# Kernel tuning notes

Hardware: AMD Instinct MI355X
Metric: run time of the kernel (lower is better)

The kernel has to match this reference:

```python
import jax, jax.numpy as jnp
import numpy as np

B, T, D = 8, 4096, 768
N_HEADS = 12
HEAD_DIM = D // N_HEADS
N_STATE = 64
ALPHA = 0.1


def setup_inputs() -> dict:
    key = jax.random.key(0)
    k1, k2, k3 = jax.random.split(key, 3)
    H = jax.random.normal(k1, (B, T, D), dtype=jnp.float32)
    prototypes = jax.random.normal(k2, (N_STATE, D), dtype=jnp.float32)
    W_tok = jax.random.normal(k3, (D, D), dtype=jnp.float32) * (1.0 / np.sqrt(D))
    s0 = jnp.zeros((1, N_STATE, D), dtype=jnp.float32)
    return {"H": H, "prototypes": prototypes, "W_tok": W_tok, "s0": s0}


def reference(H, prototypes, W_tok, s0):
    b, t, d = H.shape
    hd = HEAD_DIM
    a = ALPHA
    # q: [B, n_heads, T, head_dim]
    q = (H @ W_tok.T).reshape(b, t, N_HEADS, hd).transpose(0, 2, 1, 3)
    # k: [n_heads, n_state, head_dim]
    k = prototypes.reshape(N_STATE, N_HEADS, hd).transpose(1, 0, 2)
    # score: [B, n_heads, T, n_state]; routing_temp == 1.0
    score = jnp.einsum('bhtd,hmd->bhtm', q, k) / (hd ** 0.5)
    w = jax.nn.softmax(score, axis=-1)
    g = 1.0 - a * w
    # suffix-inclusive product over T: prod_{t'>=t} g[t']
    suffix_inc = jnp.flip(jnp.cumprod(jnp.flip(g, axis=2), axis=2), axis=2)
    suffix_exc = jnp.concatenate(
        [suffix_inc[:, :, 1:, :], jnp.ones_like(suffix_inc[:, :, :1, :])], axis=2)
    w_eff = a * w * suffix_exc  # [B, H, T, n_state]
    h_ph = H.reshape(b, t, N_HEADS, hd).transpose(0, 2, 1, 3)  # [B,H,T,hd]
    s0h = jnp.broadcast_to(s0, (b, N_STATE, d)).reshape(
        b, N_STATE, N_HEADS, hd).transpose(0, 2, 1, 3)  # [B,H,n_state,hd]
    residual = suffix_inc[:, :, 0, :][..., None]  # [B,H,n_state,1]
    s = s0h * residual + jnp.einsum('bhtm,bhtd->bhmd', w_eff, h_ph)
    return s.transpose(0, 2, 1, 3).reshape(b, N_STATE, d)
```

## Files before the change

kernel.cpp:

```cpp
#include <hip/hip_runtime.h>

#define B_ 8
#define T_ 4096
#define D_ 768
#define NH_ 12
#define M_ 64
#define ALPHA_ 0.1f

#define CCH 16
#define CHUNK_T 256

using half8 = __attribute__((ext_vector_type(8))) _Float16;
using short8 = __attribute__((ext_vector_type(8))) short;
using f32x4 = __attribute__((ext_vector_type(4))) float;

__device__ __forceinline__ unsigned int f2h2(float a, float b) {
    unsigned short ua = __builtin_bit_cast(unsigned short, (_Float16)a);
    unsigned short ub = __builtin_bit_cast(unsigned short, (_Float16)b);
    return (unsigned int)ua | ((unsigned int)ub << 16);
}
__device__ __forceinline__ float h2f(unsigned short u) {
    return (float)__builtin_bit_cast(_Float16, u);
}
__device__ __forceinline__ void gload_lds16(const void* g, void* l) {
    __builtin_amdgcn_global_load_lds(
        (const __attribute__((address_space(1))) unsigned int*)g,
        (__attribute__((address_space(3))) unsigned int*)l, 16, 0, 0);
}

__global__ __launch_bounds__(256) void kH16(const float* __restrict__ H,
                                            unsigned short* __restrict__ H16) {
    const int i = blockIdx.x * 256 + threadIdx.x;
#pragma unroll
    for (int j = 0; j < 4; ++j) {
        const int idx = i + j * 1572864;
        const float4 v = reinterpret_cast<const float4*>(H)[idx];
        uint2 pk = {f2h2(v.x, v.y), f2h2(v.z, v.w)};
        reinterpret_cast<uint2*>(H16)[idx] = pk;
    }
}

__global__ __launch_bounds__(256) void kP(const float* __restrict__ proto,
                                          const float* __restrict__ W,
                                          unsigned short* __restrict__ P16) {
    const int et = blockIdx.x;
    const int h  = blockIdx.y;
    const int tid = threadIdx.x;

    __shared__ __align__(16) float Ws[64 * 128];
    __shared__ __align__(16) float Ks[64 * 64];

#pragma unroll
    for (int j = 0; j < 8; ++j) {
        int f = tid + j * 256;
        int i = f >> 5, c4 = f & 31;
        const float4 v = *reinterpret_cast<const float4*>(
            W + (size_t)(h * 64 + i) * D_ + et * 128 + c4 * 4);
        *reinterpret_cast<float4*>(&Ws[i * 128 + c4 * 4]) = v;
    }
#pragma unroll
    for (int j = 0; j < 4; ++j) {
        int f = tid + j * 256;
        int m = f >> 4, i4 = f & 15;
        const float4 v = *reinterpret_cast<const float4*>(
            proto + (size_t)m * D_ + h * 64 + i4 * 4);
        Ks[(i4 * 4 + 0) * 64 + m] = v.x;
        Ks[(i4 * 4 + 1) * 64 + m] = v.y;
        Ks[(i4 * 4 + 2) * 64 + m] = v.z;
        Ks[(i4 * 4 + 3) * 64 + m] = v.w;
    }
    __syncthreads();

    const int m0 = (tid >> 5) * 8;
    const int e0 = (tid & 31) * 4;
    float acc[8][4];
#pragma unroll
    for (int i = 0; i < 8; ++i)
#pragma unroll
        for (int j = 0; j < 4; ++j) acc[i][j] = 0.f;

    for (int i = 0; i < 64; ++i) {
        const float4 bb = *reinterpret_cast<const float4*>(&Ws[i * 128 + e0]);
        const float4 a0 = *reinterpret_cast<const float4*>(&Ks[i * 64 + m0]);
        const float4 a1 = *reinterpret_cast<const float4*>(&Ks[i * 64 + m0 + 4]);
        const float a[8] = {a0.x, a0.y, a0.z, a0.w, a1.x, a1.y, a1.z, a1.w};
#pragma unroll
        for (int mi = 0; mi < 8; ++mi) {
            acc[mi][0] = fmaf(a[mi], bb.x, acc[mi][0]);
            acc[mi][1] = fmaf(a[mi], bb.y, acc[mi][1]);
            acc[mi][2] = fmaf(a[mi], bb.z, acc[mi][2]);
            acc[mi][3] = fmaf(a[mi], bb.w, acc[mi][3]);
        }
    }
#pragma unroll
    for (int mi = 0; mi < 8; ++mi) {
        size_t idx = (size_t)(h * 64 + m0 + mi) * D_ + et * 128 + e0;
        uint2 pk = {f2h2(acc[mi][0] * 0.125f, acc[mi][1] * 0.125f),
                    f2h2(acc[mi][2] * 0.125f, acc[mi][3] * 0.125f)};
        *reinterpret_cast<uint2*>(P16 + idx) = pk;
    }
}

#define LDS_BYTES 51712

__global__ __launch_bounds__(256, 3) void k1(const unsigned short* __restrict__ H16,
                                             const unsigned short* __restrict__ P16,
                                             float* __restrict__ chunkprod,
                                             float* __restrict__ partial) {
    const int p = blockIdx.x;
    const int b = p & 7;
    const int s = p >> 3;
    const int h = s % 12;
    const int c = s / 12;
    const int tid = threadIdx.x;
    const int wv  = tid >> 6;
    const int lane = tid & 63;
    const int l15 = lane & 15;
    const int q4  = lane >> 4;

    extern __shared__ __align__(16) unsigned char smem[];
    unsigned short* wT = (unsigned short*)(smem);
    unsigned short* Hh = (unsigned short*)(smem + 33792);
    float* segprod = (float*)(smem + 50688);

    const size_t Hrow = (size_t)(b * T_ + c * CHUNK_T);
    const unsigned short* gA = H16 + Hrow * D_;
    const unsigned short* gB = P16 + (size_t)h * 64 * D_;

    f32x4 acc[4][4] = {};

    for (int kt = 0; kt < 12; ++kt) {
        __syncthreads();
#pragma unroll
        for (int j = 0; j < 8; ++j) {
            int sl = j * 256 + tid;
            int r = sl >> 3, gp = sl & 7, g = gp ^ (r & 7);
            gload_lds16(gA + (size_t)r * D_ + kt * 64 + g * 8, smem + sl * 16);
        }
#pragma unroll
        for (int j = 0; j < 2; ++j) {
            int sl = j * 256 + tid;
            int r = sl >> 3, gp = sl & 7, g = gp ^ (r & 7);
            gload_lds16(gB + (size_t)r * D_ + kt * 64 + g * 8, smem + 32768 + sl * 16);
        }
        __syncthreads();
#pragma unroll
        for (int ks = 0; ks < 2; ++ks) {
            const int gp = ((ks * 4 + q4) ^ (l15 & 7)) * 16;
            half8 af[4], bf[4];
#pragma unroll
            for (int tt = 0; tt < 4; ++tt)
                af[tt] = *reinterpret_cast<const half8*>(
                    smem + (wv * 64 + tt * 16 + l15) * 128 + gp);
#pragma unroll
            for (int mt = 0; mt < 4; ++mt)
                bf[mt] = *reinterpret_cast<const half8*>(
                    smem + 32768 + (mt * 16 + l15) * 128 + gp);
#pragma unroll
            for (int tt = 0; tt < 4; ++tt)
#pragma unroll
                for (int mt = 0; mt < 4; ++mt)
                    acc[tt][mt] = __builtin_amdgcn_mfma_f32_16x16x32_f16(
                        af[tt], bf[mt], acc[tt][mt], 0, 0, 0);
        }
    }
    __syncthreads();

#pragma unroll
    for (int tt = 0; tt < 4; ++tt)
#pragma unroll
        for (int rg = 0; rg < 4; ++rg) {
            float mx = fmaxf(fmaxf(acc[tt][0][rg], acc[tt][1][rg]),
                             fmaxf(acc[tt][2][rg], acc[tt][3][rg]));
#pragma unroll
            for (int msk = 1; msk <= 8; msk <<= 1)
                mx = fmaxf(mx, __shfl_xor(mx, msk, 64));
            float e0 = __expf(acc[tt][0][rg] - mx);
            float e1 = __expf(acc[tt][1][rg] - mx);
            float e2 = __expf(acc[tt][2][rg] - mx);
            float e3 = __expf(acc[tt][3][rg] - mx);
            float sm = (e0 + e1) + (e2 + e3);
#pragma unroll
            for (int msk = 1; msk <= 8; msk <<= 1)
                sm += __shfl_xor(sm, msk, 64);
            float inv = 1.0f / sm;
            acc[tt][0][rg] = e0 * inv;
            acc[tt][1][rg] = e1 * inv;
            acc[tt][2][rg] = e2 * inv;
            acc[tt][3][rg] = e3 * inv;
        }
#pragma unroll
    for (int tt = 0; tt < 4; ++tt)
#pragma unroll
        for (int mt = 0; mt < 4; ++mt) {
            uint2 pk = {f2h2(acc[tt][mt][0], acc[tt][mt][1]),
                        f2h2(acc[tt][mt][2], acc[tt][mt][3])};
            *reinterpret_cast<uint2*>(
                wT + (mt * 16 + l15) * 264 + wv * 64 + tt * 16 + q4 * 4) = pk;
        }
    __syncthreads();

    {
        const int g = tid >> 6, m_s = tid & 63;
        unsigned short* rowp = wT + m_s * 264 + g * 64;
        float pband = 1.0f;
#pragma unroll
        for (int oct = 0; oct < 8; ++oct) {
            short8 v = *reinterpret_cast<const short8*>(rowp + oct * 8);
#pragma unroll
            for (int j = 0; j < 8; ++j)
                pband *= fmaf(-ALPHA_, h2f((unsigned short)v[j]), 1.0f);
        }
        segprod[m_s * 4 + g] = pband;
        __syncthreads();
        float R = 1.0f;
#pragma unroll
        for (int gg = 1; gg < 4; ++gg)
            if (g + gg < 4) R *= segprod[m_s * 4 + g + gg];
#pragma unroll
        for (int oct = 7; oct >= 0; --oct) {
            short8 v = *reinterpret_cast<const short8*>(rowp + oct * 8);
            short8 o;
#pragma unroll
            for (int j = 7; j >= 0; --j) {
                float w = h2f((unsigned short)v[j]);
                _Float16 we = (_Float16)(ALPHA_ * w * R);
                o[j] = (short)__builtin_bit_cast(unsigned short, we);
                R *= fmaf(-ALPHA_, w, 1.0f);
            }
            *reinterpret_cast<short8*>(rowp + oct * 8) = o;
        }
    }
    __syncthreads();

    f32x4 pacc[4] = {};
    for (int hf = 0; hf < 2; ++hf) {
        if (hf) __syncthreads();
        {
            const int dp = tid & 15, tg = tid >> 4;
            const unsigned short* src = H16 + (Hrow + tg * 16) * D_
                                        + h * 64 + hf * 32 + 2 * dp;
            unsigned short* dst0 = Hh + (2 * dp) * 264 + tg * 16;
            unsigned short* dst1 = Hh + (2 * dp + 1) * 264 + tg * 16;
#pragma unroll
            for (int i = 0; i < 16; ++i) {
                unsigned int v = *reinterpret_cast<const unsigned int*>(src + (size_t)i * D_);
                dst0[i] = (unsigned short)(v & 0xffffu);
                dst1[i] = (unsigned short)(v >> 16);
            }
        }
        __syncthreads();
#pragma unroll
        for (int ks = 0; ks < 8; ++ks) {
            half8 a = *reinterpret_cast<const half8*>(
                wT + (wv * 16 + l15) * 264 + ks * 32 + q4 * 8);
#pragma unroll
            for (int dt = 0; dt < 2; ++dt) {
                half8 bb = *reinterpret_cast<const half8*>(
                    Hh + (dt * 16 + l15) * 264 + ks * 32 + q4 * 8);
                pacc[hf * 2 + dt] = __builtin_amdgcn_mfma_f32_16x16x32_f16(
                    a, bb, pacc[hf * 2 + dt], 0, 0, 0);
            }
        }
    }

    const int chunkIdx = (b * NH_ + h) * CCH + c;
    if (tid < 64)
        chunkprod[(size_t)chunkIdx * 64 + tid] =
            (segprod[tid * 4 + 0] * segprod[tid * 4 + 1]) *
            (segprod[tid * 4 + 2] * segprod[tid * 4 + 3]);
#pragma unroll
    for (int dt = 0; dt < 4; ++dt)
#pragma unroll
        for (int rg = 0; rg < 4; ++rg)
            partial[((size_t)chunkIdx * 64 + wv * 16 + q4 * 4 + rg) * 64 + dt * 16 + l15] =
                pacc[dt][rg];
}

__global__ __launch_bounds__(256) void k2(const float* __restrict__ chunkprod,
                                          const float* __restrict__ partial,
                                          const float* __restrict__ s0,
                                          float* __restrict__ out) {
    const int h = blockIdx.x;
    const int b = blockIdx.y;
    const int mg = blockIdx.z;
    const int tid = threadIdx.x;
    const int m  = mg * 16 + (tid >> 4);
    const int d0 = (tid & 15) * 4;

    const size_t cpBase = (size_t)(b * NH_ + h) * CCH;
    float sfx[CCH];
    float run = 1.0f;
#pragma unroll
    for (int c = CCH - 1; c >= 0; --c) {
        sfx[c] = run;
        run *= chunkprod[(cpBase + c) * M_ + m];
    }
    const float4 v0 = *reinterpret_cast<const float4*>(
        s0 + (size_t)m * D_ + h * 64 + d0);
    float4 acc = make_float4(v0.x * run, v0.y * run, v0.z * run, v0.w * run);
#pragma unroll
    for (int c = 0; c < CCH; ++c) {
        const float sv = sfx[c];
        const float4 pp = *reinterpret_cast<const float4*>(
            partial + ((cpBase + c) * M_ + m) * 64 + d0);
        acc.x = fmaf(sv, pp.x, acc.x);
        acc.y = fmaf(sv, pp.y, acc.y);
        acc.z = fmaf(sv, pp.z, acc.z);
        acc.w = fmaf(sv, pp.w, acc.w);
    }
    *reinterpret_cast<float4*>(out + (size_t)(b * M_ + m) * D_ + h * 64 + d0) = acc;
}

extern "C" void kernel_launch(void* const* d_in, const int* in_sizes, int n_in,
                              void* d_out, int out_size, void* d_ws, size_t ws_size,
                              hipStream_t stream) {
    const float* H     = (const float*)d_in[0];
    const float* proto = (const float*)d_in[1];
    const float* W     = (const float*)d_in[2];
    const float* s0    = (const float*)d_in[3];
    float* out = (float*)d_out;

    unsigned short* H16 = (unsigned short*)d_ws;
    unsigned short* P16 = (unsigned short*)((unsigned char*)d_ws + 50331648);
    float* chunkprod = (float*)((unsigned char*)d_ws + 51511296);
    float* partial   = (float*)((unsigned char*)d_ws + 51904512);

    kH16<<<dim3(6144), 256, 0, stream>>>(H, H16);
    kP<<<dim3(6, NH_), 256, 0, stream>>>(proto, W, P16);
    k1<<<dim3(1536), 256, LDS_BYTES, stream>>>(H16, P16, chunkprod, partial);
    k2<<<dim3(NH_, B_, 4), 256, 0, stream>>>(chunkprod, partial, s0, out);
}
```

Measured before the change: 230.0 us.

## Merge prep kernels and load MFMA operands directly from global memory

The fp16 conversion of H and the prototype projection kernel are merged into one launch, with block index ranges selecting the role. In the scoring kernel, the LDS-staged tile loads (global_load_lds with swizzle and two barriers per k-tile) are replaced by direct per-lane half8 global loads feeding the MFMAs over a fully unrolled K loop. This removes LDS staging and synchronisation and one launch. In exchange each wave re-reads operands from global/L2 with strided row accesses, and the P16 tile is no longer shared through LDS.

```diff
diff --git a/kernel.cpp b/kernel.cpp
--- a/kernel.cpp
+++ b/kernel.cpp
@@ -22,33 +22,30 @@
 __device__ __forceinline__ float h2f(unsigned short u) {
     return (float)__builtin_bit_cast(_Float16, u);
 }
-__device__ __forceinline__ void gload_lds16(const void* g, void* l) {
-    __builtin_amdgcn_global_load_lds(
-        (const __attribute__((address_space(1))) unsigned int*)g,
-        (__attribute__((address_space(3))) unsigned int*)l, 16, 0, 0);
-}
-
-__global__ __launch_bounds__(256) void kH16(const float* __restrict__ H,
-                                            unsigned short* __restrict__ H16) {
-    const int i = blockIdx.x * 256 + threadIdx.x;
-#pragma unroll
-    for (int j = 0; j < 4; ++j) {
-        const int idx = i + j * 1572864;
-        const float4 v = reinterpret_cast<const float4*>(H)[idx];
-        uint2 pk = {f2h2(v.x, v.y), f2h2(v.z, v.w)};
-        reinterpret_cast<uint2*>(H16)[idx] = pk;
-    }
-}
-
-__global__ __launch_bounds__(256) void kP(const float* __restrict__ proto,
-                                          const float* __restrict__ W,
-                                          unsigned short* __restrict__ P16) {
-    const int et = blockIdx.x;
-    const int h  = blockIdx.y;
+
+__global__ __launch_bounds__(256) void kprep(const float* __restrict__ H,
+                                             const float* __restrict__ proto,
+                                             const float* __restrict__ W,
+                                             unsigned short* __restrict__ H16,
+                                             unsigned short* __restrict__ P16) {
     const int tid = threadIdx.x;
-
     __shared__ __align__(16) float Ws[64 * 128];
     __shared__ __align__(16) float Ks[64 * 64];
+
+    if (blockIdx.x < 6144) {
+        const int i = blockIdx.x * 256 + tid;
+#pragma unroll
+        for (int j = 0; j < 4; ++j) {
+            const int idx = i + j * 1572864;
+            const float4 v = reinterpret_cast<const float4*>(H)[idx];
+            uint2 pk = {f2h2(v.x, v.y), f2h2(v.z, v.w)};
+            reinterpret_cast<uint2*>(H16)[idx] = pk;
+        }
+        return;
+    }
+    const int r  = blockIdx.x - 6144;
+    const int et = r % 6;
+    const int h  = r / 6;
 
 #pragma unroll
     for (int j = 0; j < 8; ++j) {
@@ -124,47 +121,27 @@
     float* segprod = (float*)(smem + 50688);
 
     const size_t Hrow = (size_t)(b * T_ + c * CHUNK_T);
-    const unsigned short* gA = H16 + Hrow * D_;
-    const unsigned short* gB = P16 + (size_t)h * 64 * D_;
+
+    const unsigned short* aB = H16 + (Hrow + wv * 64 + l15) * D_ + q4 * 8;
+    const unsigned short* bB = P16 + ((size_t)h * 64 + l15) * D_ + q4 * 8;
 
     f32x4 acc[4][4] = {};
-
-    for (int kt = 0; kt < 12; ++kt) {
-        __syncthreads();
-#pragma unroll
-        for (int j = 0; j < 8; ++j) {
-            int sl = j * 256 + tid;
-            int r = sl >> 3, gp = sl & 7, g = gp ^ (r & 7);
-            gload_lds16(gA + (size_t)r * D_ + kt * 64 + g * 8, smem + sl * 16);
-        }
-#pragma unroll
-        for (int j = 0; j < 2; ++j) {
-            int sl = j * 256 + tid;
-            int r = sl >> 3, gp = sl & 7, g = gp ^ (r & 7);
-            gload_lds16(gB + (size_t)r * D_ + kt * 64 + g * 8, smem + 32768 + sl * 16);
-        }
-        __syncthreads();
-#pragma unroll
-        for (int ks = 0; ks < 2; ++ks) {
-            const int gp = ((ks * 4 + q4) ^ (l15 & 7)) * 16;
-            half8 af[4], bf[4];
-#pragma unroll
-            for (int tt = 0; tt < 4; ++tt)
-                af[tt] = *reinterpret_cast<const half8*>(
-                    smem + (wv * 64 + tt * 16 + l15) * 128 + gp);
+#pragma unroll
+    for (int ks = 0; ks < 24; ++ks) {
+        half8 af[4], bf[4];
+#pragma unroll
+        for (int tt = 0; tt < 4; ++tt)
+            af[tt] = *reinterpret_cast<const half8*>(aB + (size_t)tt * 16 * D_ + ks * 32);
+#pragma unroll
+        for (int mt = 0; mt < 4; ++mt)
+            bf[mt] = *reinterpret_cast<const half8*>(bB + (size_t)mt * 16 * D_ + ks * 32);
+#pragma unroll
+        for (int tt = 0; tt < 4; ++tt)
 #pragma unroll
             for (int mt = 0; mt < 4; ++mt)
-                bf[mt] = *reinterpret_cast<const half8*>(
-                    smem + 32768 + (mt * 16 + l15) * 128 + gp);
-#pragma unroll
-            for (int tt = 0; tt < 4; ++tt)
-#pragma unroll
-                for (int mt = 0; mt < 4; ++mt)
-                    acc[tt][mt] = __builtin_amdgcn_mfma_f32_16x16x32_f16(
-                        af[tt], bf[mt], acc[tt][mt], 0, 0, 0);
-        }
-    }
-    __syncthreads();
+                acc[tt][mt] = __builtin_amdgcn_mfma_f32_16x16x32_f16(
+                    af[tt], bf[mt], acc[tt][mt], 0, 0, 0);
+    }
 
 #pragma unroll
     for (int tt = 0; tt < 4; ++tt)
@@ -326,8 +303,7 @@
     float* chunkprod = (float*)((unsigned char*)d_ws + 51511296);
     float* partial   = (float*)((unsigned char*)d_ws + 51904512);
 
-    kH16<<<dim3(6144), 256, 0, stream>>>(H, H16);
-    kP<<<dim3(6, NH_), 256, 0, stream>>>(proto, W, P16);
+    kprep<<<dim3(6216), 256, 0, stream>>>(H, proto, W, H16, P16);
     k1<<<dim3(1536), 256, LDS_BYTES, stream>>>(H16, P16, chunkprod, partial);
     k2<<<dim3(NH_, B_, 4), 256, 0, stream>>>(chunkprod, partial, s0, out);
 }
```

New measurement: 310.4 us. +35.0%, slower.

## Merge prep kernels and fold chunk reduction into k1 via last-block counter

Applied to the files above, without the earlier changes.

Merges the fp16 conversion of H and the prototype projection into one launch by splitting the grid on block index. The separate k2 combine kernel is removed: each k1 block bumps an atomic counter per (batch, head), and the last of the 16 chunk blocks performs the suffix-product combine and writes the output. This cuts two kernel launches and their gaps, at the cost of threadfences, an atomic per block, and a serialized tail done by one block per (b,h). Counters are zeroed inside the prep kernel, which relies on stream ordering.

```diff
diff --git a/kernel.cpp b/kernel.cpp
--- a/kernel.cpp
+++ b/kernel.cpp
@@ -28,27 +28,31 @@
         (__attribute__((address_space(3))) unsigned int*)l, 16, 0, 0);
 }
 
-__global__ __launch_bounds__(256) void kH16(const float* __restrict__ H,
-                                            unsigned short* __restrict__ H16) {
-    const int i = blockIdx.x * 256 + threadIdx.x;
-#pragma unroll
-    for (int j = 0; j < 4; ++j) {
-        const int idx = i + j * 1572864;
-        const float4 v = reinterpret_cast<const float4*>(H)[idx];
-        uint2 pk = {f2h2(v.x, v.y), f2h2(v.z, v.w)};
-        reinterpret_cast<uint2*>(H16)[idx] = pk;
-    }
-}
-
-__global__ __launch_bounds__(256) void kP(const float* __restrict__ proto,
-                                          const float* __restrict__ W,
-                                          unsigned short* __restrict__ P16) {
-    const int et = blockIdx.x;
-    const int h  = blockIdx.y;
+__global__ __launch_bounds__(256) void kprep(const float* __restrict__ H,
+                                             const float* __restrict__ proto,
+                                             const float* __restrict__ W,
+                                             unsigned short* __restrict__ H16,
+                                             unsigned short* __restrict__ P16,
+                                             unsigned int* __restrict__ counters) {
     const int tid = threadIdx.x;
-
     __shared__ __align__(16) float Ws[64 * 128];
     __shared__ __align__(16) float Ks[64 * 64];
+
+    if (blockIdx.x < 6144) {
+        const int i = blockIdx.x * 256 + tid;
+#pragma unroll
+        for (int j = 0; j < 4; ++j) {
+            const int idx = i + j * 1572864;
+            const float4 v = reinterpret_cast<const float4*>(H)[idx];
+            uint2 pk = {f2h2(v.x, v.y), f2h2(v.z, v.w)};
+            reinterpret_cast<uint2*>(H16)[idx] = pk;
+        }
+        return;
+    }
+    const int r  = blockIdx.x - 6144;
+    if (r == 0 && tid < 96) counters[tid] = 0u;
+    const int et = r % 6;
+    const int h  = r / 6;
 
 #pragma unroll
     for (int j = 0; j < 8; ++j) {
@@ -105,8 +109,11 @@
 
 __global__ __launch_bounds__(256, 3) void k1(const unsigned short* __restrict__ H16,
                                              const unsigned short* __restrict__ P16,
+                                             const float* __restrict__ s0,
                                              float* __restrict__ chunkprod,
-                                             float* __restrict__ partial) {
+                                             float* __restrict__ partial,
+                                             unsigned int* __restrict__ counters,
+                                             float* __restrict__ out) {
     const int p = blockIdx.x;
     const int b = p & 7;
     const int s = p >> 3;
@@ -122,6 +129,7 @@
     unsigned short* wT = (unsigned short*)(smem);
     unsigned short* Hh = (unsigned short*)(smem + 33792);
     float* segprod = (float*)(smem + 50688);
+    __shared__ int isLast;
 
     const size_t Hrow = (size_t)(b * T_ + c * CHUNK_T);
     const unsigned short* gA = H16 + Hrow * D_;
@@ -134,14 +142,14 @@
 #pragma unroll
         for (int j = 0; j < 8; ++j) {
             int sl = j * 256 + tid;
-            int r = sl >> 3, gp = sl & 7, g = gp ^ (r & 7);
-            gload_lds16(gA + (size_t)r * D_ + kt * 64 + g * 8, smem + sl * 16);
+            int rr = sl >> 3, gp = sl & 7, g = gp ^ (rr & 7);
+            gload_lds16(gA + (size_t)rr * D_ + kt * 64 + g * 8, smem + sl * 16);
         }
 #pragma unroll
         for (int j = 0; j < 2; ++j) {
             int sl = j * 256 + tid;
-            int r = sl >> 3, gp = sl & 7, g = gp ^ (r & 7);
-            gload_lds16(gB + (size_t)r * D_ + kt * 64 + g * 8, smem + 32768 + sl * 16);
+            int rr = sl >> 3, gp = sl & 7, g = gp ^ (rr & 7);
+            gload_lds16(gB + (size_t)rr * D_ + kt * 64 + g * 8, smem + 32768 + sl * 16);
         }
         __syncthreads();
 #pragma unroll
@@ -264,7 +272,8 @@
         }
     }
 
-    const int chunkIdx = (b * NH_ + h) * CCH + c;
+    const int bh = b * NH_ + h;
+    const int chunkIdx = bh * CCH + c;
     if (tid < 64)
         chunkprod[(size_t)chunkIdx * 64 + tid] =
             (segprod[tid * 4 + 0] * segprod[tid * 4 + 1]) *
@@ -275,41 +284,47 @@
         for (int rg = 0; rg < 4; ++rg)
             partial[((size_t)chunkIdx * 64 + wv * 16 + q4 * 4 + rg) * 64 + dt * 16 + l15] =
                 pacc[dt][rg];
-}
-
-__global__ __launch_bounds__(256) void k2(const float* __restrict__ chunkprod,
-                                          const float* __restrict__ partial,
-                                          const float* __restrict__ s0,
-                                          float* __restrict__ out) {
-    const int h = blockIdx.x;
-    const int b = blockIdx.y;
-    const int mg = blockIdx.z;
-    const int tid = threadIdx.x;
-    const int m  = mg * 16 + (tid >> 4);
-    const int d0 = (tid & 15) * 4;
-
-    const size_t cpBase = (size_t)(b * NH_ + h) * CCH;
-    float sfx[CCH];
-    float run = 1.0f;
-#pragma unroll
-    for (int c = CCH - 1; c >= 0; --c) {
-        sfx[c] = run;
-        run *= chunkprod[(cpBase + c) * M_ + m];
-    }
-    const float4 v0 = *reinterpret_cast<const float4*>(
-        s0 + (size_t)m * D_ + h * 64 + d0);
-    float4 acc = make_float4(v0.x * run, v0.y * run, v0.z * run, v0.w * run);
-#pragma unroll
-    for (int c = 0; c < CCH; ++c) {
-        const float sv = sfx[c];
-        const float4 pp = *reinterpret_cast<const float4*>(
-            partial + ((cpBase + c) * M_ + m) * 64 + d0);
-        acc.x = fmaf(sv, pp.x, acc.x);
-        acc.y = fmaf(sv, pp.y, acc.y);
-        acc.z = fmaf(sv, pp.z, acc.z);
-        acc.w = fmaf(sv, pp.w, acc.w);
-    }
-    *reinterpret_cast<float4*>(out + (size_t)(b * M_ + m) * D_ + h * 64 + d0) = acc;
+
+    __threadfence();
+    if (tid == 0)
+        isLast = (atomicAdd(&counters[bh], 1u) == CCH - 1) ? 1 : 0;
+    __syncthreads();
+    if (isLast) {
+        __threadfence();
+        const size_t cpBase = (size_t)bh * CCH;
+        const int m  = tid >> 2;
+        const int d0 = (tid & 3) * 16;
+        float sfx[CCH];
+        float run = 1.0f;
+#pragma unroll
+        for (int c2 = CCH - 1; c2 >= 0; --c2) {
+            sfx[c2] = run;
+            run *= chunkprod[(cpBase + c2) * M_ + m];
+        }
+        float4 acc4[4];
+#pragma unroll
+        for (int qq = 0; qq < 4; ++qq) {
+            const float4 v = *reinterpret_cast<const float4*>(
+                s0 + (size_t)m * D_ + h * 64 + d0 + qq * 4);
+            acc4[qq] = make_float4(v.x * run, v.y * run, v.z * run, v.w * run);
+        }
+        for (int c2 = 0; c2 < CCH; ++c2) {
+            const float sv = sfx[c2];
+            const size_t base = ((cpBase + c2) * M_ + m) * 64 + d0;
+#pragma unroll
+            for (int qq = 0; qq < 4; ++qq) {
+                const float4 pp = *reinterpret_cast<const float4*>(partial + base + qq * 4);
+                acc4[qq].x = fmaf(sv, pp.x, acc4[qq].x);
+                acc4[qq].y = fmaf(sv, pp.y, acc4[qq].y);
+                acc4[qq].z = fmaf(sv, pp.z, acc4[qq].z);
+                acc4[qq].w = fmaf(sv, pp.w, acc4[qq].w);
+            }
+        }
+        const size_t ob = (size_t)(b * M_ + m) * D_ + h * 64 + d0;
+#pragma unroll
+        for (int qq = 0; qq < 4; ++qq)
+            *reinterpret_cast<float4*>(out + ob + qq * 4) = acc4[qq];
+    }
 }
 
 extern "C" void kernel_launch(void* const* d_in, const int* in_sizes, int n_in,
@@ -325,9 +340,9 @@
     unsigned short* P16 = (unsigned short*)((unsigned char*)d_ws + 50331648);
     float* chunkprod = (float*)((unsigned char*)d_ws + 51511296);
     float* partial   = (float*)((unsigned char*)d_ws + 51904512);
-
-    kH16<<<dim3(6144), 256, 0, stream>>>(H, H16);
-    kP<<<dim3(6, NH_), 256, 0, stream>>>(proto, W, P16);
-    k1<<<dim3(1536), 256, LDS_BYTES, stream>>>(H16, P16, chunkprod, partial);
-    k2<<<dim3(NH_, B_, 4), 256, 0, stream>>>(chunkprod, partial, s0, out);
-}
+    unsigned int* counters = (unsigned int*)((unsigned char*)d_ws + 77070336);
+
+    kprep<<<dim3(6216), 256, 0, stream>>>(H, proto, W, H16, P16, counters);
+    k1<<<dim3(1536), 256, LDS_BYTES, stream>>>(H16, P16, s0, chunkprod, partial,
+                                               counters, out);
+}
```

Measured after the change: 418.7 us. 82.1% more time.

## Fuse fp32-to-fp16 conversion of H into the main GEMM kernel

Applied to the files above, without the earlier changes.

Removes the separate kernel that converted H to fp16 into a workspace buffer. The main kernel now reads fp32 H straight into LDS, converting to half in registers before the MFMA and when staging the per-head slice for the second matmul. This drops one full write and re-read of a 50MB intermediate and one launch. In exchange each K step moves twice the bytes into LDS, the K loop runs twice as many iterations with a sync each, and the new LDS layout gives up the XOR swizzle, so bank conflicts may appear.

```diff
diff --git a/kernel.cpp b/kernel.cpp
--- a/kernel.cpp
+++ b/kernel.cpp
@@ -22,22 +22,18 @@
 __device__ __forceinline__ float h2f(unsigned short u) {
     return (float)__builtin_bit_cast(_Float16, u);
 }
+__device__ __forceinline__ half8 cvt8(float4 a, float4 b) {
+    half8 r;
+    r[0] = (_Float16)a.x; r[1] = (_Float16)a.y;
+    r[2] = (_Float16)a.z; r[3] = (_Float16)a.w;
+    r[4] = (_Float16)b.x; r[5] = (_Float16)b.y;
+    r[6] = (_Float16)b.z; r[7] = (_Float16)b.w;
+    return r;
+}
 __device__ __forceinline__ void gload_lds16(const void* g, void* l) {
     __builtin_amdgcn_global_load_lds(
         (const __attribute__((address_space(1))) unsigned int*)g,
         (__attribute__((address_space(3))) unsigned int*)l, 16, 0, 0);
-}
-
-__global__ __launch_bounds__(256) void kH16(const float* __restrict__ H,
-                                            unsigned short* __restrict__ H16) {
-    const int i = blockIdx.x * 256 + threadIdx.x;
-#pragma unroll
-    for (int j = 0; j < 4; ++j) {
-        const int idx = i + j * 1572864;
-        const float4 v = reinterpret_cast<const float4*>(H)[idx];
-        uint2 pk = {f2h2(v.x, v.y), f2h2(v.z, v.w)};
-        reinterpret_cast<uint2*>(H16)[idx] = pk;
-    }
 }
 
 __global__ __launch_bounds__(256) void kP(const float* __restrict__ proto,
@@ -103,7 +99,7 @@
 
 #define LDS_BYTES 51712
 
-__global__ __launch_bounds__(256, 3) void k1(const unsigned short* __restrict__ H16,
+__global__ __launch_bounds__(256, 3) void k1(const float* __restrict__ H,
                                              const unsigned short* __restrict__ P16,
                                              float* __restrict__ chunkprod,
                                              float* __restrict__ partial) {
@@ -124,45 +120,41 @@
     float* segprod = (float*)(smem + 50688);
 
     const size_t Hrow = (size_t)(b * T_ + c * CHUNK_T);
-    const unsigned short* gA = H16 + Hrow * D_;
+    const float* gA = H + Hrow * D_;
     const unsigned short* gB = P16 + (size_t)h * 64 * D_;
 
     f32x4 acc[4][4] = {};
 
-    for (int kt = 0; kt < 12; ++kt) {
+    for (int kt = 0; kt < 24; ++kt) {
         __syncthreads();
 #pragma unroll
-        for (int j = 0; j < 8; ++j) {
-            int sl = j * 256 + tid;
-            int r = sl >> 3, gp = sl & 7, g = gp ^ (r & 7);
-            gload_lds16(gA + (size_t)r * D_ + kt * 64 + g * 8, smem + sl * 16);
-        }
-#pragma unroll
-        for (int j = 0; j < 2; ++j) {
-            int sl = j * 256 + tid;
-            int r = sl >> 3, gp = sl & 7, g = gp ^ (r & 7);
-            gload_lds16(gB + (size_t)r * D_ + kt * 64 + g * 8, smem + 32768 + sl * 16);
-        }
+        for (int j = 0; j < 8; ++j)
+            gload_lds16(gA + (size_t)tid * D_ + kt * 32 + j * 4,
+                        smem + (j * 256 + tid) * 16);
+        gload_lds16(gB + (size_t)(tid & 63) * D_ + kt * 32 + (tid >> 6) * 8,
+                    smem + 32768 + tid * 16);
         __syncthreads();
-#pragma unroll
-        for (int ks = 0; ks < 2; ++ks) {
-            const int gp = ((ks * 4 + q4) ^ (l15 & 7)) * 16;
-            half8 af[4], bf[4];
-#pragma unroll
-            for (int tt = 0; tt < 4; ++tt)
-                af[tt] = *reinterpret_cast<const half8*>(
-                    smem + (wv * 64 + tt * 16 + l15) * 128 + gp);
+
+        half8 af[4], bf[4];
+#pragma unroll
+        for (int tt = 0; tt < 4; ++tt) {
+            const int row = wv * 64 + tt * 16 + l15;
+            const float4 lo = *reinterpret_cast<const float4*>(
+                smem + ((2 * q4) * 256 + row) * 16);
+            const float4 hi = *reinterpret_cast<const float4*>(
+                smem + ((2 * q4 + 1) * 256 + row) * 16);
+            af[tt] = cvt8(lo, hi);
+        }
+#pragma unroll
+        for (int mt = 0; mt < 4; ++mt)
+            bf[mt] = *reinterpret_cast<const half8*>(
+                smem + 32768 + (q4 * 64 + mt * 16 + l15) * 16);
+#pragma unroll
+        for (int tt = 0; tt < 4; ++tt)
 #pragma unroll
             for (int mt = 0; mt < 4; ++mt)
-                bf[mt] = *reinterpret_cast<const half8*>(
-                    smem + 32768 + (mt * 16 + l15) * 128 + gp);
-#pragma unroll
-            for (int tt = 0; tt < 4; ++tt)
-#pragma unroll
-                for (int mt = 0; mt < 4; ++mt)
-                    acc[tt][mt] = __builtin_amdgcn_mfma_f32_16x16x32_f16(
-                        af[tt], bf[mt], acc[tt][mt], 0, 0, 0);
-        }
+                acc[tt][mt] = __builtin_amdgcn_mfma_f32_16x16x32_f16(
+                    af[tt], bf[mt], acc[tt][mt], 0, 0, 0);
     }
     __syncthreads();
 
@@ -237,16 +229,15 @@
     for (int hf = 0; hf < 2; ++hf) {
         if (hf) __syncthreads();
         {
-            const int dp = tid & 15, tg = tid >> 4;
-            const unsigned short* src = H16 + (Hrow + tg * 16) * D_
-                                        + h * 64 + hf * 32 + 2 * dp;
-            unsigned short* dst0 = Hh + (2 * dp) * 264 + tg * 16;
-            unsigned short* dst1 = Hh + (2 * dp + 1) * 264 + tg * 16;
-#pragma unroll
-            for (int i = 0; i < 16; ++i) {
-                unsigned int v = *reinterpret_cast<const unsigned int*>(src + (size_t)i * D_);
-                dst0[i] = (unsigned short)(v & 0xffffu);
-                dst1[i] = (unsigned short)(v >> 16);
+            const int dl = tid & 31, tg = tid >> 5;
+            const float* src = H + Hrow * D_ + (size_t)(tg * 32) * D_
+                               + h * 64 + hf * 32 + dl;
+            unsigned short* dst = Hh + dl * 264 + tg * 32;
+#pragma unroll
+            for (int i = 0; i < 32; i += 2) {
+                float a  = src[(size_t)i * D_];
+                float bb = src[(size_t)(i + 1) * D_];
+                *reinterpret_cast<unsigned int*>(dst + i) = f2h2(a, bb);
             }
         }
         __syncthreads();
@@ -321,13 +312,11 @@
     const float* s0    = (const float*)d_in[3];
     float* out = (float*)d_out;
 
-    unsigned short* H16 = (unsigned short*)d_ws;
-    unsigned short* P16 = (unsigned short*)((unsigned char*)d_ws + 50331648);
-    float* chunkprod = (float*)((unsigned char*)d_ws + 51511296);
-    float* partial   = (float*)((unsigned char*)d_ws + 51904512);
-
-    kH16<<<dim3(6144), 256, 0, stream>>>(H, H16);
+    unsigned short* P16 = (unsigned short*)d_ws;
+    float* chunkprod = (float*)((unsigned char*)d_ws + 1179648);
+    float* partial   = (float*)((unsigned char*)d_ws + 1572864);
+
     kP<<<dim3(6, NH_), 256, 0, stream>>>(proto, W, P16);
-    k1<<<dim3(1536), 256, LDS_BYTES, stream>>>(H16, P16, chunkprod, partial);
+    k1<<<dim3(1536), 256, LDS_BYTES, stream>>>(H, P16, chunkprod, partial);
     k2<<<dim3(NH_, B_, 4), 256, 0, stream>>>(chunkprod, partial, s0, out);
 }
```

Result: slower. 374.0 us (+62.6%).
